# Optimization experiments

Hardware: AMD Instinct MI355X
Metric: run time of the kernel (lower is better)

The kernel has to match this reference:

```python
import jax, jax.numpy as jnp
import numpy as np
from jax import lax

B, T, C, H = 4, 2048, 1024, 16
K = C // H            # head size = 64
E_MIX, E_DEC = 32, 64  # TIME_MIX_EXTRA_DIM, TIME_DECAY_EXTRA_DIM
EPS = 1e-5 * 8**2      # GroupNorm eps with head_size_divisor=8


def setup_inputs() -> dict:
    key = jax.random.key(0)
    ks = jax.random.split(key, 24)
    u01 = lambda k, s: jax.random.uniform(k, s, jnp.float32, -0.01, 0.01)
    nrm = lambda k, s, sc: jax.random.normal(k, s, jnp.float32) * sc
    return {
        "x": jax.random.normal(ks[0], (B, T, C), jnp.float32),
        "time_maa_x": jax.random.uniform(ks[1], (1, 1, C)),
        "time_maa_w": jax.random.uniform(ks[2], (1, 1, C)),
        "time_maa_k": jax.random.uniform(ks[3], (1, 1, C)),
        "time_maa_v": jax.random.uniform(ks[4], (1, 1, C)),
        "time_maa_r": jax.random.uniform(ks[5], (1, 1, C)),
        "time_maa_g": jax.random.uniform(ks[6], (1, 1, C)),
        "maa_w1": u01(ks[7], (C, 5 * E_MIX)),
        "maa_w2": u01(ks[8], (5, E_MIX, C)),
        "time_decay": jax.random.uniform(ks[9], (1, 1, C), jnp.float32, -6.0, -1.0),
        "td_w1": u01(ks[10], (C, E_DEC)),
        "td_w2": u01(ks[11], (E_DEC, C)),
        "u": nrm(ks[12], (H, K), 0.1),   # time_faaaa
        "Wr": nrm(ks[13], (C, C), 0.02),
        "Wk": nrm(ks[14], (C, C), 0.02),
        "Wv": nrm(ks[15], (C, C), 0.02),
        "Wg": nrm(ks[16], (C, C), 0.02),
        "Wo": nrm(ks[17], (C, C), 0.02),
        "ln_g": jnp.ones((C,), jnp.float32),
        "ln_b": jnp.zeros((C,), jnp.float32),
    }


def _rwkv6_tmix(x, time_maa_x, time_maa_w, time_maa_k, time_maa_v, time_maa_r,
                time_maa_g, maa_w1, maa_w2, time_decay, td_w1, td_w2, u,
                Wr, Wk, Wv, Wg, Wo, ln_g, ln_b):
    b, t, c = x.shape
    # token shift: prepend zero row, drop last (ZeroPad2d((0,0,1,-1)))
    x_prev = jnp.pad(x, ((0, 0), (1, 0), (0, 0)))[:, :t]
    xx = x_prev - x
    # low-rank data-dependent mixing
    mix = jnp.tanh((x + xx * time_maa_x) @ maa_w1).reshape(b, t, 5, E_MIX)
    mix = jnp.einsum('btfe,fec->fbtc', mix, maa_w2)  # [5,B,T,C]
    mw, mk, mv, mr, mg = mix
    xw = x + xx * (time_maa_w + mw)
    xk = x + xx * (time_maa_k + mk)
    xv = x + xx * (time_maa_v + mv)
    xr = x + xx * (time_maa_r + mr)
    xg = x + xx * (time_maa_g + mg)
    r = xr @ Wr.T
    k = xk @ Wk.T
    v = xv @ Wv.T
    g = jax.nn.silu(xg @ Wg.T)
    w = time_decay + jnp.tanh(xw @ td_w1) @ td_w2
    decay = jnp.exp(-jnp.exp(w))  # per-channel decay in (0,1)

    # WKV6 linear recurrence, scan over time, vectorized over (B,H)
    to_tbhk = lambda a: a.reshape(b, t, H, K).transpose(1, 0, 2, 3)
    rs, ks_, vs, ds = map(to_tbhk, (r, k, v, decay))

    def step(S, inp):  # S: [B,H,K,K] (key x value)
        r_t, k_t, v_t, d_t = inp
        kv = k_t[..., :, None] * v_t[..., None, :]          # [B,H,K,K]
        y = jnp.einsum('bhk,bhkj->bhj', r_t, S + u[None, :, :, None] * kv)
        S = d_t[..., None] * S + kv
        return S, y

    S0 = jnp.zeros((b, H, K, K), x.dtype)
    _, y = lax.scan(step, S0, (rs, ks_, vs, ds))            # y: [T,B,H,K]
    y = y.transpose(1, 0, 2, 3)                             # [B,T,H,K]

    # GroupNorm over each head's K channels
    mu = y.mean(-1, keepdims=True)
    var = y.var(-1, keepdims=True)
    y = ((y - mu) / jnp.sqrt(var + EPS)).reshape(b, t, c) * ln_g + ln_b
    return (y * g) @ Wo.T


def reference(x, time_maa_x, time_maa_w, time_maa_k, time_maa_v, time_maa_r,
              time_maa_g, maa_w1, maa_w2, time_decay, td_w1, td_w2, u,
              Wr, Wk, Wv, Wg, Wo, ln_g, ln_b):
    return _rwkv6_tmix(x, time_maa_x, time_maa_w, time_maa_k, time_maa_v,
                       time_maa_r, time_maa_g, maa_w1, maa_w2, time_decay,
                       td_w1, td_w2, u, Wr, Wk, Wv, Wg, Wo, ln_g, ln_b)
```

## Files before the change

kernel.cpp:

```cpp
#include <hip/hip_runtime.h>

typedef unsigned int u32;
typedef unsigned short u16;
typedef __attribute__((ext_vector_type(8))) short short8;
typedef __attribute__((ext_vector_type(4))) float f32x4;

__device__ __forceinline__ float b2f(u16 h){ u32 x = ((u32)h) << 16; return __builtin_bit_cast(float, x); }
__device__ __forceinline__ u16 f2b(float f){
  u32 x = __builtin_bit_cast(u32, f);
  x += 0x7fffu + ((x >> 16) & 1u);
  return (u16)(x >> 16);
}
#define LOH(u) ((u16)((u) & 0xffffu))
#define HIH(u) ((u16)((u) >> 16))

__device__ __forceinline__ void gload16(const u16* g, u16* lds){
  __builtin_amdgcn_global_load_lds((const __attribute__((address_space(1))) u32*)g,
                                   (__attribute__((address_space(3))) u32*)lds, 16, 0, 0);
}

struct G4P { const u16* A[5]; const u16* B[5]; u16* C[5]; };

template<int MODE>
__global__ __launch_bounds__(256, 4) void gemm128_k(G4P gp, float* __restrict__ Cf)
{
  __shared__ u16 lds[16384];
  const int tid = threadIdx.x;
  const int z = blockIdx.z;
  if (MODE == 0 && z == 4 && blockIdx.y != 0) return;
  const u16* __restrict__ A  = gp.A[z];
  const u16* __restrict__ Bw = gp.B[z];
  const int wid = tid >> 6, lane = tid & 63;
  const int wr = wid >> 1, wc = wid & 1;
  const int l16 = lane & 15, kq = lane >> 4;
  const int swr = (l16 >> 1) & 3;
  const long row0 = (long)blockIdx.x * 128;
  const long col0 = (long)blockIdx.y * 128;

  f32x4 acc[4][4];
#pragma unroll
  for (int i = 0; i < 4; i++)
#pragma unroll
    for (int j = 0; j < 4; j++) acc[i][j] = (f32x4)0.0f;

  const int srow = tid >> 2;
  const int sk8 = ((tid & 3) ^ ((tid >> 3) & 3)) * 8;
  const u16* Agp = A  + (row0 + srow) * 1024 + sk8;
  const u16* Bgp = Bw + (col0 + srow) * 1024 + sk8;

  auto STAGE = [&](int buf, int kt){
    u16* Ab = lds + buf * 8192;
    u16* Bb = Ab + 4096;
    const int ko = kt * 32;
    gload16(Agp + ko,         Ab + tid * 8);
    gload16(Agp + 65536 + ko, Ab + (tid + 256) * 8);
    gload16(Bgp + ko,         Bb + tid * 8);
    gload16(Bgp + 65536 + ko, Bb + (tid + 256) * 8);
  };

  STAGE(0, 0);
  const int NT = 32;
  for (int t = 0; t < NT; t++){
    const int cur = t & 1;
    if (t + 1 < NT){
      STAGE(cur ^ 1, t + 1);
      asm volatile("s_waitcnt vmcnt(4)" ::: "memory");
    } else {
      asm volatile("s_waitcnt vmcnt(0)" ::: "memory");
    }
    __builtin_amdgcn_sched_barrier(0);
    __builtin_amdgcn_s_barrier();
    __builtin_amdgcn_sched_barrier(0);
    const u16* Ab = lds + cur * 8192;
    const u16* Bb = Ab + 4096;
    short8 afr[4], bfr[4];
#pragma unroll
    for (int ni = 0; ni < 4; ni++)
      bfr[ni] = *(const short8*)&Bb[(wc*64 + ni*16 + l16)*32 + (kq ^ swr)*8];
#pragma unroll
    for (int mi = 0; mi < 4; mi++)
      afr[mi] = *(const short8*)&Ab[(wr*64 + mi*16 + l16)*32 + (kq ^ swr)*8];
    __builtin_amdgcn_s_setprio(1);
#pragma unroll
    for (int mi = 0; mi < 4; mi++)
#pragma unroll
      for (int ni = 0; ni < 4; ni++)
        acc[mi][ni] = __builtin_amdgcn_mfma_f32_16x16x32_bf16(afr[mi], bfr[ni], acc[mi][ni], 0, 0, 0);
    __builtin_amdgcn_s_setprio(0);
    __builtin_amdgcn_s_barrier();
  }

  const bool SILU = (MODE == 0) && (z == 3);
  const bool TANH = (MODE == 0) && (z == 4);
  const int  ldc  = (MODE == 0 && z == 4) ? 128 : 1024;
#pragma unroll
  for (int mi = 0; mi < 4; mi++){
#pragma unroll
    for (int qq = 0; qq < 4; qq++){
      const long r = row0 + wr*64 + mi*16 + kq*4 + qq;
      if (MODE == 0){
        u16* crow = gp.C[z] + r * ldc + col0 + wc*64 + l16;
#pragma unroll
        for (int ni = 0; ni < 4; ni++){
          float v = acc[mi][ni][qq];
          if (SILU) v = v / (1.0f + expf(-v));
          if (TANH) v = tanhf(v);
          crow[ni * 16] = f2b(v);
        }
      } else {
        float* crow = Cf + r * 1024 + col0 + wc*64 + l16;
#pragma unroll
        for (int ni = 0; ni < 4; ni++)
          crow[ni * 16] = acc[mi][ni][qq];
      }
    }
  }
}

__global__ __launch_bounds__(256) void gemm_tanh(
    const u16* __restrict__ A, int lda,
    const u16* __restrict__ B, int ldb,
    u16* __restrict__ C, int ldc, int K)
{
  __shared__ u16 As[4096];
  __shared__ u16 Bs[4096];
  const int tid = threadIdx.x;
  const int wave = tid >> 6, lane = tid & 63;
  const int wr = wave >> 1, wc = wave & 1;
  const int l16 = lane & 15, kq = lane >> 4;
  const long row0 = (long)blockIdx.x * 128;
  const long col0 = (long)blockIdx.y * 128;

  f32x4 acc[4][4];
#pragma unroll
  for (int i = 0; i < 4; i++)
#pragma unroll
    for (int j = 0; j < 4; j++) acc[i][j] = (f32x4)0.0f;

  const int c0 = tid, c1 = tid + 256;
  const u16* Ag0 = A + (row0 + (c0 >> 2)) * (long)lda + (c0 & 3) * 8;
  const u16* Ag1 = A + (row0 + (c1 >> 2)) * (long)lda + (c1 & 3) * 8;
  const u16* Bg0 = B + (col0 + (c0 >> 2)) * (long)ldb + (c0 & 3) * 8;
  const u16* Bg1 = B + (col0 + (c1 >> 2)) * (long)ldb + (c1 & 3) * 8;
  u16* Al0 = &As[c0 * 8]; u16* Al1 = &As[c1 * 8];
  u16* Bl0 = &Bs[c0 * 8]; u16* Bl1 = &Bs[c1 * 8];

  for (int kk = 0; kk < K; kk += 32){
    __syncthreads();
    gload16(Ag0 + kk, Al0);
    gload16(Ag1 + kk, Al1);
    gload16(Bg0 + kk, Bl0);
    gload16(Bg1 + kk, Bl1);
    __syncthreads();
    short8 af[4], bfr[4];
#pragma unroll
    for (int mi = 0; mi < 4; mi++) af[mi]  = *(const short8*)&As[(wr*64 + mi*16 + l16)*32 + kq*8];
#pragma unroll
    for (int ni = 0; ni < 4; ni++) bfr[ni] = *(const short8*)&Bs[(wc*64 + ni*16 + l16)*32 + kq*8];
#pragma unroll
    for (int mi = 0; mi < 4; mi++)
#pragma unroll
      for (int ni = 0; ni < 4; ni++)
        acc[mi][ni] = __builtin_amdgcn_mfma_f32_16x16x32_bf16(af[mi], bfr[ni], acc[mi][ni], 0, 0, 0);
  }

#pragma unroll
  for (int mi = 0; mi < 4; mi++){
#pragma unroll
    for (int qq = 0; qq < 4; qq++){
      const long r = row0 + wr*64 + mi*16 + kq*4 + qq;
#pragma unroll
      for (int ni = 0; ni < 4; ni++){
        const long c = col0 + wc*64 + ni*16 + l16;
        C[r * ldc + c] = f2b(tanhf(acc[mi][ni][qq]));
      }
    }
  }
}

struct Mix5P { const u32* pxx; u16* out[5]; const float* tm[5]; };

__global__ __launch_bounds__(256) void gemm_mix5(
    const u16* __restrict__ Am, const u16* __restrict__ W2T, Mix5P mp)
{
  __shared__ u16 As[128 * 160];
  __shared__ u16 Bs[128 * 32];
  const int tid = threadIdx.x;
  const int wave = tid >> 6, lane = tid & 63;
  const int wr = wave >> 1, wc = wave & 1;
  const int l16 = lane & 15, kq = lane >> 4;
  const long row0 = (long)blockIdx.x * 128;
  const long col0 = (long)blockIdx.y * 128;

#pragma unroll
  for (int it = 0; it < 10; it++){
    const int c = tid + it * 256;
    const int r = c / 20, c8 = c - r * 20;
    gload16(Am + (row0 + r) * 256 + c8 * 8, &As[c * 8]);
  }

  u32 pxx[64];
#pragma unroll
  for (int mi = 0; mi < 4; mi++)
#pragma unroll
    for (int qq = 0; qq < 4; qq++){
      const long r = row0 + wr*64 + mi*16 + kq*4 + qq;
#pragma unroll
      for (int ni = 0; ni < 4; ni++){
        const long c = col0 + wc*64 + ni*16 + l16;
        pxx[mi*16 + qq*4 + ni] = mp.pxx[r * 1024 + c];
      }
    }

  for (int z = 0; z < 5; z++){
    __syncthreads();
    const u16* B = W2T + z * 32768;
#pragma unroll
    for (int it = 0; it < 2; it++){
      const int c = tid + it * 256;
      gload16(B + (col0 + (c >> 2)) * 32 + (c & 3) * 8, &Bs[c * 8]);
    }
    __syncthreads();
    short8 af[4], bfr[4];
#pragma unroll
    for (int mi = 0; mi < 4; mi++) af[mi]  = *(const short8*)&As[(wr*64 + mi*16 + l16)*160 + z*32 + kq*8];
#pragma unroll
    for (int ni = 0; ni < 4; ni++) bfr[ni] = *(const short8*)&Bs[(wc*64 + ni*16 + l16)*32 + kq*8];
    f32x4 acc[4][4];
#pragma unroll
    for (int i = 0; i < 4; i++)
#pragma unroll
      for (int j = 0; j < 4; j++) acc[i][j] = (f32x4)0.0f;
#pragma unroll
    for (int mi = 0; mi < 4; mi++)
#pragma unroll
      for (int ni = 0; ni < 4; ni++)
        acc[mi][ni] = __builtin_amdgcn_mfma_f32_16x16x32_bf16(af[mi], bfr[ni], acc[mi][ni], 0, 0, 0);

    const float* tm = mp.tm[z];
    float tmv[4];
#pragma unroll
    for (int ni = 0; ni < 4; ni++) tmv[ni] = tm[col0 + wc*64 + ni*16 + l16];
    u16* C = mp.out[z];
#pragma unroll
    for (int mi = 0; mi < 4; mi++){
#pragma unroll
      for (int qq = 0; qq < 4; qq++){
        const long r = row0 + wr*64 + mi*16 + kq*4 + qq;
        u16* crow = C + r * 1024 + col0 + wc*64 + l16;
#pragma unroll
        for (int ni = 0; ni < 4; ni++){
          const u32 pk = pxx[mi*16 + qq*4 + ni];
          const float xc = b2f(LOH(pk));
          const float xx = b2f(HIH(pk));
          crow[ni * 16] = f2b(xc + xx * (tmv[ni] + acc[mi][ni][qq]));
        }
      }
    }
  }
}

__global__ __launch_bounds__(256) void mkxm_k(const float* __restrict__ X,
    const float* __restrict__ tmx, u16* __restrict__ XM, u32* __restrict__ PXX)
{
  const long idx = (long)blockIdx.x * 256 + threadIdx.x;
  const long m = idx >> 8;
  const int c4 = (int)(idx & 255) * 4;
  const float4 x = *(const float4*)(X + m * 1024 + c4);
  float4 p = make_float4(0.f, 0.f, 0.f, 0.f);
  if ((m & 2047) != 0) p = *(const float4*)(X + (m - 1) * 1024 + c4);
  const float4 t = *(const float4*)(tmx + c4);
  ushort4 o;
  o.x = f2b(x.x + (p.x - x.x) * t.x);
  o.y = f2b(x.y + (p.y - x.y) * t.y);
  o.z = f2b(x.z + (p.z - x.z) * t.z);
  o.w = f2b(x.w + (p.w - x.w) * t.w);
  *(ushort4*)(XM + m * 1024 + c4) = o;
  uint4 px;
  px.x = (u32)f2b(x.x) | ((u32)f2b(p.x - x.x) << 16);
  px.y = (u32)f2b(x.y) | ((u32)f2b(p.y - x.y) << 16);
  px.z = (u32)f2b(x.z) | ((u32)f2b(p.z - x.z) << 16);
  px.w = (u32)f2b(x.w) | ((u32)f2b(p.w - x.w) << 16);
  *(uint4*)(PXX + m * 1024 + c4) = px;
}

struct PrepP { const float* s[5]; u16* d[5];
               const float* mw1; const float* mw2; const float* tdw1; const float* tdw2;
               u16* w1t; u16* w2t; u16* tw1t; u16* tw2t; };
__global__ __launch_bounds__(256) void prep_k(PrepP pp)
{
  const int y = blockIdx.y;
  const long idx = (long)blockIdx.x * 256 + threadIdx.x;
  if (y < 5){
    const float4 v = ((const float4*)pp.s[y])[idx];
    ushort4 o; o.x = f2b(v.x); o.y = f2b(v.y); o.z = f2b(v.z); o.w = f2b(v.w);
    ((ushort4*)pp.d[y])[idx] = o;
  } else if (y == 5){
    const int k = (int)(idx & 1023);
    const int n = (int)(idx >> 10);
    pp.w1t[idx] = (n < 160) ? f2b(pp.mw1[(long)k * 160 + n]) : (u16)0;
  } else if (y == 6){
    if (idx >= 163840) return;
    const int k = (int)(idx & 31);
    const int col = (int)(idx >> 5) & 1023;
    const int f = (int)(idx >> 15);
    pp.w2t[idx] = f2b(pp.mw2[f * 32768 + k * 1024 + col]);
  } else if (y == 7){
    if (idx >= 131072) return;
    const int k = (int)(idx & 1023);
    const int n = (int)(idx >> 10);
    pp.tw1t[idx] = (n < 64) ? f2b(pp.tdw1[(long)k * 64 + n]) : (u16)0;
  } else {
    if (idx >= 65536) return;
    const int k = (int)(idx & 63);
    const int n = (int)(idx >> 6);
    pp.tw2t[idx] = f2b(pp.tdw2[(long)k * 1024 + n]);
  }
}

__global__ __launch_bounds__(256) void wkv_s1(
    u16* __restrict__ Rg, const u16* __restrict__ Kg, const u16* __restrict__ Vg,
    const u16* __restrict__ Hbg, const u16* __restrict__ TW2Tg,
    const float* __restrict__ TDg, const float* __restrict__ Ug,
    u16* __restrict__ Yg, float* __restrict__ Ag, float* __restrict__ Pg)
{
  __shared__ u16 RT_[64 * 72];
  __shared__ u16 KT_[64 * 72];
  __shared__ u16 KTT_[64 * 72];
  __shared__ u16 V_[64 * 72];
  __shared__ u16 VT_[64 * 72];
  __shared__ char UD_[64 * 68 * 4];
  __shared__ float us_[64];
  __shared__ float td_[64];
  __shared__ float dg4_[256];
  __shared__ float dg_[64];
  float* D_ = (float*)UD_;
  u16*  M_  = (u16*)UD_;

  const int tid = threadIdx.x;
  const int bh = blockIdx.x >> 5, ch = blockIdx.x & 31;
  const int b = bh >> 4, h = bh & 15, cb = h * 64;
  const long rowb = (long)b * 2048 + ch * 64;

  if (tid < 64){ us_[tid] = Ug[cb + tid]; td_[tid] = TDg[cb + tid]; }

  const int iS = tid >> 2, sg = tid & 3;
  {
    const uint4* hsrc = (const uint4*)(Hbg + (rowb + iS) * 128 + sg * 16);
    uint4* hdst = (uint4*)&RT_[iS * 72 + sg * 16];
    hdst[0] = hsrc[0]; hdst[1] = hsrc[1];
    const uint4* wsrc = (const uint4*)(TW2Tg + (cb + iS) * 64 + sg * 16);
    uint4* wdst = (uint4*)&KT_[iS * 72 + sg * 16];
    wdst[0] = wsrc[0]; wdst[1] = wsrc[1];
  }
  __syncthreads();
  {
    const int wave = tid >> 6, lane = tid & 63;
    const int wr = wave >> 1, wc = wave & 1;
    const int l16 = lane & 15, kq = lane >> 4;
    f32x4 dacc[2][2];
#pragma unroll
    for (int a = 0; a < 2; a++)
#pragma unroll
      for (int c = 0; c < 2; c++) dacc[a][c] = (f32x4)0.0f;
#pragma unroll
    for (int ks = 0; ks < 2; ks++){
      short8 af[2], bf[2];
#pragma unroll
      for (int mi = 0; mi < 2; mi++) af[mi] = *(const short8*)&RT_[(wr*32 + mi*16 + l16)*72 + ks*32 + kq*8];
#pragma unroll
      for (int ni = 0; ni < 2; ni++) bf[ni] = *(const short8*)&KT_[(wc*32 + ni*16 + l16)*72 + ks*32 + kq*8];
#pragma unroll
      for (int mi = 0; mi < 2; mi++)
#pragma unroll
        for (int ni = 0; ni < 2; ni++)
          dacc[mi][ni] = __builtin_amdgcn_mfma_f32_16x16x32_bf16(af[mi], bf[ni], dacc[mi][ni], 0, 0, 0);
    }
    __syncthreads();
#pragma unroll
    for (int mi = 0; mi < 2; mi++)
#pragma unroll
      for (int ni = 0; ni < 2; ni++)
#pragma unroll
        for (int qq = 0; qq < 4; qq++){
          const int ii = wr*32 + mi*16 + kq*4 + qq;
          const int jj = wc*32 + ni*16 + l16;
          D_[ii * 68 + jj] = expf(-expf(dacc[mi][ni][qq] + td_[jj]));
        }
  }
  {
    const long go = (rowb + iS) * 1024 + cb + sg * 16;
    uint4 a0 = *(const uint4*)(Rg + go);
    uint4 a1 = *(const uint4*)(Rg + go + 8);
    u32* rd = (u32*)&RT_[iS * 72 + sg * 16];
    rd[0]=a0.x; rd[1]=a0.y; rd[2]=a0.z; rd[3]=a0.w;
    rd[4]=a1.x; rd[5]=a1.y; rd[6]=a1.z; rd[7]=a1.w;
    a0 = *(const uint4*)(Kg + go); a1 = *(const uint4*)(Kg + go + 8);
    u32* kd = (u32*)&KT_[iS * 72 + sg * 16];
    kd[0]=a0.x; kd[1]=a0.y; kd[2]=a0.z; kd[3]=a0.w;
    kd[4]=a1.x; kd[5]=a1.y; kd[6]=a1.z; kd[7]=a1.w;
    a0 = *(const uint4*)(Vg + go); a1 = *(const uint4*)(Vg + go + 8);
    u32* vd = (u32*)&V_[iS * 72 + sg * 16];
    vd[0]=a0.x; vd[1]=a0.y; vd[2]=a0.z; vd[3]=a0.w;
    vd[4]=a1.x; vd[5]=a1.y; vd[6]=a1.z; vd[7]=a1.w;
    const u32 vw[8] = {a0.x,a0.y,a0.z,a0.w,a1.x,a1.y,a1.z,a1.w};
#pragma unroll
    for (int e = 0; e < 8; e++){
      VT_[(sg*16 + 2*e    ) * 72 + iS] = LOH(vw[e]);
      VT_[(sg*16 + 2*e + 1) * 72 + iS] = HIH(vw[e]);
    }
  }
  __syncthreads();
  {
    const int i = tid & 63, q = tid >> 6;
    const u32* rr = (const u32*)&RT_[i * 72 + q * 16];
    const u32* kr = (const u32*)&KT_[i * 72 + q * 16];
    const float* up = &us_[q * 16];
    float ds = 0.0f;
#pragma unroll
    for (int e = 0; e < 8; e++){
      ds += b2f(LOH(rr[e])) * up[2*e]   * b2f(LOH(kr[e]));
      ds += b2f(HIH(rr[e])) * up[2*e+1] * b2f(HIH(kr[e]));
    }
    dg4_[i * 4 + q] = ds;
  }
  __syncthreads();
  if (tid < 64){
    const int k = tid;
    dg_[k] = dg4_[k*4] + dg4_[k*4+1] + dg4_[k*4+2] + dg4_[k*4+3];
    float pz = 1.0f;
#pragma unroll 4
    for (int i = 0; i < 64; i++){
      const float d = D_[i * 68 + k];
      const int ro = i * 72 + k;
      RT_[ro] = f2b(b2f(RT_[ro]) * pz);
      pz *= d;
      const u16 kb = f2b(b2f(KT_[ro]) * (1.0f / pz));
      KT_[ro] = kb;
      KTT_[k * 72 + i] = kb;
    }
    Pg[((long)bh * 32 + ch) * 64 + k] = pz;
  }
  __syncthreads();
  {
    const u32* rr = (const u32*)&RT_[iS * 72 + sg * 16];
    u32* out = (u32*)(Rg + (rowb + iS) * 1024 + cb + sg * 16);
#pragma unroll
    for (int e = 0; e < 8; e++) out[e] = rr[e];
  }
  const int wave = tid >> 6, lane = tid & 63;
  const int wr = wave >> 1, wc = wave & 1;
  const int l16 = lane & 15, kq = lane >> 4;
  {
    f32x4 acc[2][2];
#pragma unroll
    for (int a = 0; a < 2; a++)
#pragma unroll
      for (int c = 0; c < 2; c++) acc[a][c] = (f32x4)0.0f;
#pragma unroll
    for (int ks = 0; ks < 2; ks++){
      short8 af[2], bf[2];
#pragma unroll
      for (int mi = 0; mi < 2; mi++) af[mi] = *(const short8*)&RT_[(wr*32 + mi*16 + l16)*72 + ks*32 + kq*8];
#pragma unroll
      for (int ni = 0; ni < 2; ni++) bf[ni] = *(const short8*)&KT_[(wc*32 + ni*16 + l16)*72 + ks*32 + kq*8];
#pragma unroll
      for (int mi = 0; mi < 2; mi++)
#pragma unroll
        for (int ni = 0; ni < 2; ni++)
          acc[mi][ni] = __builtin_amdgcn_mfma_f32_16x16x32_bf16(af[mi], bf[ni], acc[mi][ni], 0, 0, 0);
    }
    __syncthreads();
#pragma unroll
    for (int mi = 0; mi < 2; mi++)
#pragma unroll
      for (int ni = 0; ni < 2; ni++)
#pragma unroll
        for (int qq = 0; qq < 4; qq++){
          const int ii = wr*32 + mi*16 + kq*4 + qq;
          const int ss = wc*32 + ni*16 + l16;
          M_[ii * 72 + ss] = f2b(ss < ii ? acc[mi][ni][qq] : 0.0f);
        }
  }
  __syncthreads();
  {
    f32x4 accY[2][2], accA[2][2];
#pragma unroll
    for (int a = 0; a < 2; a++)
#pragma unroll
      for (int c = 0; c < 2; c++){ accY[a][c] = (f32x4)0.0f; accA[a][c] = (f32x4)0.0f; }
#pragma unroll
    for (int ks = 0; ks < 2; ks++){
      short8 am[2], ak[2], bv[2];
#pragma unroll
      for (int mi = 0; mi < 2; mi++){
        am[mi] = *(const short8*)&M_[(wr*32 + mi*16 + l16)*72 + ks*32 + kq*8];
        ak[mi] = *(const short8*)&KTT_[(wr*32 + mi*16 + l16)*72 + ks*32 + kq*8];
      }
#pragma unroll
      for (int ni = 0; ni < 2; ni++) bv[ni] = *(const short8*)&VT_[(wc*32 + ni*16 + l16)*72 + ks*32 + kq*8];
#pragma unroll
      for (int mi = 0; mi < 2; mi++)
#pragma unroll
        for (int ni = 0; ni < 2; ni++){
          accY[mi][ni] = __builtin_amdgcn_mfma_f32_16x16x32_bf16(am[mi], bv[ni], accY[mi][ni], 0, 0, 0);
          accA[mi][ni] = __builtin_amdgcn_mfma_f32_16x16x32_bf16(ak[mi], bv[ni], accA[mi][ni], 0, 0, 0);
        }
    }
    float* abase = Ag + ((long)bh * 32 + ch) * 4096;
#pragma unroll
    for (int mi = 0; mi < 2; mi++)
#pragma unroll
      for (int qq = 0; qq < 4; qq++){
        const int ii = wr*32 + mi*16 + kq*4 + qq;
        u16* yrow = Yg + (rowb + ii) * 1024 + cb;
        float* arow = abase + ii * 64;
#pragma unroll
        for (int ni = 0; ni < 2; ni++){
          const int jj = wc*32 + ni*16 + l16;
          const float yv = accY[mi][ni][qq] + dg_[ii] * b2f(V_[ii * 72 + jj]);
          yrow[jj] = f2b(yv);
          arow[jj] = accA[mi][ni][qq];
        }
      }
  }
}

__global__ __launch_bounds__(256) void wkv_s2(
    const float* __restrict__ Ag, const float* __restrict__ Pg, float* __restrict__ Sg)
{
  const int tid = threadIdx.x;
  const int bh = blockIdx.x >> 2, kq = blockIdx.x & 3;
  const int kk = tid >> 4, jo = tid & 15;
  const int krow = kq * 16 + kk;
  const long base = (long)bh * 32;
  float4 S = make_float4(0.f, 0.f, 0.f, 0.f);
  for (int g = 0; g < 4; g++){
    float4 a[8]; float ps[8];
#pragma unroll
    for (int j = 0; j < 8; j++){
      const long c = base + g * 8 + j;
      a[j]  = *(const float4*)(Ag + c * 4096 + krow * 64 + jo * 4);
      ps[j] = Pg[c * 64 + krow];
    }
#pragma unroll
    for (int j = 0; j < 8; j++){
      const long mo = (base + g * 8 + j) * 4096 + krow * 64 + jo * 4;
      *(float4*)(Sg + mo) = S;
      S.x = ps[j] * (S.x + a[j].x); S.y = ps[j] * (S.y + a[j].y);
      S.z = ps[j] * (S.z + a[j].z); S.w = ps[j] * (S.w + a[j].w);
    }
  }
}

__global__ __launch_bounds__(256) void wkv_s3g(
    const u16* __restrict__ Rtg, const float* __restrict__ Sg,
    const u16* __restrict__ Yg, const u16* __restrict__ G,
    const float* __restrict__ lng, const float* __restrict__ lnb,
    u16* __restrict__ Z)
{
  __shared__ float Ss[4096];
  __shared__ u16 RTs[64 * 66];
  __shared__ float red1[256], red2[256];
  const int tid = threadIdx.x;
  const int bh = blockIdx.x >> 5, ch = blockIdx.x & 31;
  const int b = bh >> 4, h = bh & 15, cb = h * 64;
  const long rowb = (long)b * 2048 + ch * 64;
  const bool CROSS = (ch != 0);

  if (CROSS){
    const float4* sp = (const float4*)(Sg + ((long)bh * 32 + ch) * 4096);
    float4* sd = (float4*)Ss;
#pragma unroll
    for (int e = 0; e < 4; e++) sd[tid + e * 256] = sp[tid + e * 256];
    const int iS = tid >> 2, sg4 = tid & 3;
    const u32* src = (const u32*)(Rtg + (rowb + iS) * 1024 + cb + sg4 * 16);
    u32* dst = (u32*)&RTs[iS * 66 + sg4 * 16];
#pragma unroll
    for (int e = 0; e < 8; e++) dst[e] = src[e];
  }
  __syncthreads();

  const int i_ = tid & 63, q = tid >> 6, jb = q * 16;
  float y[16];
  {
    const u32* yp = (const u32*)(Yg + (rowb + i_) * 1024 + cb + jb);
#pragma unroll
    for (int j2 = 0; j2 < 8; j2++){
      const u32 u = yp[j2];
      y[2*j2] = b2f(LOH(u)); y[2*j2+1] = b2f(HIH(u));
    }
  }
  if (CROSS){
    float rt[64];
    const u32* rr = (const u32*)&RTs[i_ * 66];
#pragma unroll
    for (int kk = 0; kk < 32; kk++){
      const u32 u = rr[kk];
      rt[2*kk] = b2f(LOH(u)); rt[2*kk+1] = b2f(HIH(u));
    }
#pragma unroll
    for (int k = 0; k < 64; k++){
      const float rk = rt[k];
      const float4* sr = (const float4*)&Ss[k * 64 + jb];
#pragma unroll
      for (int j4 = 0; j4 < 4; j4++){
        const float4 sv = sr[j4];
        y[4*j4+0] += rk*sv.x; y[4*j4+1] += rk*sv.y; y[4*j4+2] += rk*sv.z; y[4*j4+3] += rk*sv.w;
      }
    }
  }
  float s = 0.0f, sq = 0.0f;
#pragma unroll
  for (int j = 0; j < 16; j++){ s += y[j]; sq += y[j]*y[j]; }
  red1[q * 64 + i_] = s;
  red2[q * 64 + i_] = sq;
  __syncthreads();
  const float St = red1[i_] + red1[64 + i_] + red1[128 + i_] + red1[192 + i_];
  const float Qt = red2[i_] + red2[64 + i_] + red2[128 + i_] + red2[192 + i_];
  const float mean = St * 0.015625f;
  const float var = Qt * 0.015625f - mean * mean;
  const float rstd = rsqrtf(var + 6.4e-4f);

  const u32* gp = (const u32*)(G + (rowb + i_) * 1024 + cb + jb);
  const float4* lgp = (const float4*)(lng + cb + jb);
  const float4* lbp = (const float4*)(lnb + cb + jb);
  u32* zo = (u32*)(Z + (rowb + i_) * 1024 + cb + jb);
#pragma unroll
  for (int j4 = 0; j4 < 4; j4++){
    const float4 lg = lgp[j4];
    const float4 lb = lbp[j4];
    const u32 g01 = gp[2*j4], g23 = gp[2*j4+1];
    const float z0 = ((y[4*j4+0]-mean)*rstd*lg.x + lb.x) * b2f(LOH(g01));
    const float z1 = ((y[4*j4+1]-mean)*rstd*lg.y + lb.y) * b2f(HIH(g01));
    const float z2 = ((y[4*j4+2]-mean)*rstd*lg.z + lb.z) * b2f(LOH(g23));
    const float z3 = ((y[4*j4+3]-mean)*rstd*lg.w + lb.w) * b2f(HIH(g23));
    zo[2*j4]   = (u32)f2b(z0) | ((u32)f2b(z1) << 16);
    zo[2*j4+1] = (u32)f2b(z2) | ((u32)f2b(z3) << 16);
  }
}

extern "C" void kernel_launch(void* const* d_in, const int* in_sizes, int n_in,
                              void* d_out, int out_size, void* d_ws, size_t ws_size,
                              hipStream_t stream)
{
  (void)in_sizes; (void)n_in; (void)out_size; (void)ws_size;
  const float* X    = (const float*)d_in[0];
  const float* TMX  = (const float*)d_in[1];
  const float* TMW  = (const float*)d_in[2];
  const float* TMK  = (const float*)d_in[3];
  const float* TMV  = (const float*)d_in[4];
  const float* TMR  = (const float*)d_in[5];
  const float* TMG  = (const float*)d_in[6];
  const float* MW1  = (const float*)d_in[7];
  const float* MW2  = (const float*)d_in[8];
  const float* TD   = (const float*)d_in[9];
  const float* TDW1 = (const float*)d_in[10];
  const float* TDW2 = (const float*)d_in[11];
  const float* U    = (const float*)d_in[12];
  const float* WR   = (const float*)d_in[13];
  const float* WK   = (const float*)d_in[14];
  const float* WV   = (const float*)d_in[15];
  const float* WG   = (const float*)d_in[16];
  const float* WO   = (const float*)d_in[17];
  const float* LNG  = (const float*)d_in[18];
  const float* LNB  = (const float*)d_in[19];

  char* ws = (char*)d_ws;
  const size_t SLOT = 16777216ULL;
  u16* S1 = (u16*)(ws + 0 * SLOT);
  u16* S2 = (u16*)(ws + 1 * SLOT);
  u16* S3 = (u16*)(ws + 2 * SLOT);
  u16* S4 = (u16*)(ws + 3 * SLOT);
  u16* S5 = (u16*)(ws + 4 * SLOT);
  u16* S6 = (u16*)(ws + 5 * SLOT);
  u16* S7 = (u16*)(ws + 6 * SLOT);
  u16* S8 = (u16*)(ws + 7 * SLOT);
  u16* S9 = (u16*)(ws + 8 * SLOT);
  char* p = ws + 9 * SLOT;
  auto alloc = [&](size_t bytes) -> void* {
    void* q = p; p += (bytes + 255) & ~(size_t)255; return q;
  };
  u16* MIXB = (u16*)alloc(8192ULL * 256 * 2);
  u16* Hb   = (u16*)alloc(8192ULL * 128 * 2);
  u16* W1T  = (u16*)alloc(256ULL * 1024 * 2);
  u16* W2T  = (u16*)alloc(5ULL * 1024 * 32 * 2);
  u16* TW1T = (u16*)alloc(128ULL * 1024 * 2);
  u16* TW2T = (u16*)alloc(1024ULL * 64 * 2);
  u16* WRb  = (u16*)alloc(1048576ULL * 2);
  u16* WKb  = (u16*)alloc(1048576ULL * 2);
  u16* WVb  = (u16*)alloc(1048576ULL * 2);
  u16* WGb  = (u16*)alloc(1048576ULL * 2);
  u16* WOb  = (u16*)alloc(1048576ULL * 2);
  float* Ab = (float*)alloc(33554432ULL);
  float* Pg = (float*)alloc(524288ULL);

  u16*   XM = S1; u16* XW = S2; u16* XK = S3; u16* XV = S4; u16* XR = S5; u16* XG = S6;
  u32*   PXX = (u32*)S7;
  u16*   Rb = S1; u16* Kb = S7; u16* Vb = S8; u16* Gb = S9;
  u16*   Y   = S2;
  float* Sg  = (float*)S7;
  u16*   Z   = S4;

  PrepP pp;
  pp.s[0]=WR; pp.s[1]=WK; pp.s[2]=WV; pp.s[3]=WG; pp.s[4]=WO;
  pp.d[0]=WRb; pp.d[1]=WKb; pp.d[2]=WVb; pp.d[3]=WGb; pp.d[4]=WOb;
  pp.mw1 = MW1; pp.mw2 = MW2; pp.tdw1 = TDW1; pp.tdw2 = TDW2;
  pp.w1t = W1T; pp.w2t = W2T; pp.tw1t = TW1T; pp.tw2t = TW2T;
  prep_k<<<dim3(1024, 9), 256, 0, stream>>>(pp);

  mkxm_k<<<8192, 256, 0, stream>>>(X, TMX, XM, PXX);

  gemm_tanh<<<dim3(64, 2), 256, 0, stream>>>(XM, 1024, W1T, 1024, MIXB, 256, 1024);

  Mix5P mp;
  mp.pxx = PXX;
  mp.out[0]=XW; mp.out[1]=XK; mp.out[2]=XV; mp.out[3]=XR; mp.out[4]=XG;
  mp.tm[0]=TMW; mp.tm[1]=TMK; mp.tm[2]=TMV; mp.tm[3]=TMR; mp.tm[4]=TMG;
  gemm_mix5<<<dim3(64, 8), 256, 0, stream>>>(MIXB, W2T, mp);

  G4P gp;
  gp.A[0]=XR; gp.A[1]=XK; gp.A[2]=XV; gp.A[3]=XG; gp.A[4]=XW;
  gp.B[0]=WRb; gp.B[1]=WKb; gp.B[2]=WVb; gp.B[3]=WGb; gp.B[4]=TW1T;
  gp.C[0]=Rb; gp.C[1]=Kb; gp.C[2]=Vb; gp.C[3]=Gb; gp.C[4]=Hb;
  gemm128_k<0><<<dim3(64, 8, 5), 256, 0, stream>>>(gp, nullptr);

  wkv_s1<<<2048, 256, 0, stream>>>(Rb, Kb, Vb, Hb, TW2T, TD, U, Y, Ab, Pg);
  wkv_s2<<<256, 256, 0, stream>>>(Ab, Pg, Sg);
  wkv_s3g<<<2048, 256, 0, stream>>>(Rb, Sg, Y, Gb, LNG, LNB, Z);

  G4P go;
  go.A[0]=Z; go.B[0]=WOb; go.C[0]=nullptr;
  gemm128_k<1><<<dim3(64, 8, 1), 256, 0, stream>>>(go, (float*)d_out);
}
```

Before: 288.1 us.

## Merge weight prep with token-shift kernel and parallelize decay cumprod across waves

Folds the token-shift/mix kernel into the weight-conversion prep kernel as extra grid rows, removing one launch and letting the two independent workloads share the GPU. In wkv_s1, the serial 64-step decay cumulative product that ran on only 64 threads is split into four 16-step segments handled by all 256 threads, with segment prefix products exchanged through shared memory. This shortens the serial critical path per block at the cost of an extra barrier and a small shared buffer, and changes float rounding order slightly.

Result: faster. 275.0 us (-4.5%).

```diff
diff --git a/kernel.cpp b/kernel.cpp
--- a/kernel.cpp
+++ b/kernel.cpp
@@ -260,62 +260,61 @@
   }
 }
 
-__global__ __launch_bounds__(256) void mkxm_k(const float* __restrict__ X,
-    const float* __restrict__ tmx, u16* __restrict__ XM, u32* __restrict__ PXX)
+struct PrepMkP { const float* s[5]; u16* d[5];
+                 const float* mw1; const float* mw2; const float* tdw1; const float* tdw2;
+                 u16* w1t; u16* w2t; u16* tw1t; u16* tw2t;
+                 const float* X; const float* tmx; u16* XM; u32* PXX; };
+__global__ __launch_bounds__(256) void prepmk_k(PrepMkP pp)
 {
-  const long idx = (long)blockIdx.x * 256 + threadIdx.x;
+  const int y = blockIdx.y;
+  if (y < 9){
+    const long idx = (long)blockIdx.x * 256 + threadIdx.x;
+    if (y < 5){
+      const float4 v = ((const float4*)pp.s[y])[idx];
+      ushort4 o; o.x = f2b(v.x); o.y = f2b(v.y); o.z = f2b(v.z); o.w = f2b(v.w);
+      ((ushort4*)pp.d[y])[idx] = o;
+    } else if (y == 5){
+      const int k = (int)(idx & 1023);
+      const int n = (int)(idx >> 10);
+      pp.w1t[idx] = (n < 160) ? f2b(pp.mw1[(long)k * 160 + n]) : (u16)0;
+    } else if (y == 6){
+      if (idx >= 163840) return;
+      const int k = (int)(idx & 31);
+      const int col = (int)(idx >> 5) & 1023;
+      const int f = (int)(idx >> 15);
+      pp.w2t[idx] = f2b(pp.mw2[f * 32768 + k * 1024 + col]);
+    } else if (y == 7){
+      if (idx >= 131072) return;
+      const int k = (int)(idx & 1023);
+      const int n = (int)(idx >> 10);
+      pp.tw1t[idx] = (n < 64) ? f2b(pp.tdw1[(long)k * 64 + n]) : (u16)0;
+    } else {
+      if (idx >= 65536) return;
+      const int k = (int)(idx & 63);
+      const int n = (int)(idx >> 6);
+      pp.tw2t[idx] = f2b(pp.tdw2[(long)k * 1024 + n]);
+    }
+    return;
+  }
+  const long idx = (((long)(y - 9) * 1024 + blockIdx.x) * 256 + threadIdx.x);
   const long m = idx >> 8;
   const int c4 = (int)(idx & 255) * 4;
-  const float4 x = *(const float4*)(X + m * 1024 + c4);
+  const float4 x = *(const float4*)(pp.X + m * 1024 + c4);
   float4 p = make_float4(0.f, 0.f, 0.f, 0.f);
-  if ((m & 2047) != 0) p = *(const float4*)(X + (m - 1) * 1024 + c4);
-  const float4 t = *(const float4*)(tmx + c4);
+  if ((m & 2047) != 0) p = *(const float4*)(pp.X + (m - 1) * 1024 + c4);
+  const float4 t = *(const float4*)(pp.tmx + c4);
   ushort4 o;
   o.x = f2b(x.x + (p.x - x.x) * t.x);
   o.y = f2b(x.y + (p.y - x.y) * t.y);
   o.z = f2b(x.z + (p.z - x.z) * t.z);
   o.w = f2b(x.w + (p.w - x.w) * t.w);
-  *(ushort4*)(XM + m * 1024 + c4) = o;
+  *(ushort4*)(pp.XM + m * 1024 + c4) = o;
   uint4 px;
   px.x = (u32)f2b(x.x) | ((u32)f2b(p.x - x.x) << 16);
   px.y = (u32)f2b(x.y) | ((u32)f2b(p.y - x.y) << 16);
   px.z = (u32)f2b(x.z) | ((u32)f2b(p.z - x.z) << 16);
   px.w = (u32)f2b(x.w) | ((u32)f2b(p.w - x.w) << 16);
-  *(uint4*)(PXX + m * 1024 + c4) = px;
-}
-
-struct PrepP { const float* s[5]; u16* d[5];
-               const float* mw1; const float* mw2; const float* tdw1; const float* tdw2;
-               u16* w1t; u16* w2t; u16* tw1t; u16* tw2t; };
-__global__ __launch_bounds__(256) void prep_k(PrepP pp)
-{
-  const int y = blockIdx.y;
-  const long idx = (long)blockIdx.x * 256 + threadIdx.x;
-  if (y < 5){
-    const float4 v = ((const float4*)pp.s[y])[idx];
-    ushort4 o; o.x = f2b(v.x); o.y = f2b(v.y); o.z = f2b(v.z); o.w = f2b(v.w);
-    ((ushort4*)pp.d[y])[idx] = o;
-  } else if (y == 5){
-    const int k = (int)(idx & 1023);
-    const int n = (int)(idx >> 10);
-    pp.w1t[idx] = (n < 160) ? f2b(pp.mw1[(long)k * 160 + n]) : (u16)0;
-  } else if (y == 6){
-    if (idx >= 163840) return;
-    const int k = (int)(idx & 31);
-    const int col = (int)(idx >> 5) & 1023;
-    const int f = (int)(idx >> 15);
-    pp.w2t[idx] = f2b(pp.mw2[f * 32768 + k * 1024 + col]);
-  } else if (y == 7){
-    if (idx >= 131072) return;
-    const int k = (int)(idx & 1023);
-    const int n = (int)(idx >> 10);
-    pp.tw1t[idx] = (n < 64) ? f2b(pp.tdw1[(long)k * 64 + n]) : (u16)0;
-  } else {
-    if (idx >= 65536) return;
-    const int k = (int)(idx & 63);
-    const int n = (int)(idx >> 6);
-    pp.tw2t[idx] = f2b(pp.tdw2[(long)k * 1024 + n]);
-  }
+  *(uint4*)(pp.PXX + m * 1024 + c4) = px;
 }
 
 __global__ __launch_bounds__(256) void wkv_s1(
@@ -334,6 +333,7 @@
   __shared__ float td_[64];
   __shared__ float dg4_[256];
   __shared__ float dg_[64];
+  __shared__ float segp_[256];
   float* D_ = (float*)UD_;
   u16*  M_  = (u16*)UD_;
 
@@ -425,21 +425,29 @@
     dg4_[i * 4 + q] = ds;
   }
   __syncthreads();
-  if (tid < 64){
-    const int k = tid;
-    dg_[k] = dg4_[k*4] + dg4_[k*4+1] + dg4_[k*4+2] + dg4_[k*4+3];
+  {
+    const int k = tid & 63, seg = tid >> 6;
+    if (seg == 0) dg_[k] = dg4_[k*4] + dg4_[k*4+1] + dg4_[k*4+2] + dg4_[k*4+3];
+    const int i0 = seg * 16;
+    float lp = 1.0f;
+#pragma unroll
+    for (int i = 0; i < 16; i++) lp *= D_[(i0 + i) * 68 + k];
+    segp_[seg * 64 + k] = lp;
+    __syncthreads();
     float pz = 1.0f;
-#pragma unroll 4
-    for (int i = 0; i < 64; i++){
-      const float d = D_[i * 68 + k];
-      const int ro = i * 72 + k;
+    for (int s = 0; s < seg; s++) pz *= segp_[s * 64 + k];
+#pragma unroll
+    for (int i = 0; i < 16; i++){
+      const int ii = i0 + i;
+      const float d = D_[ii * 68 + k];
+      const int ro = ii * 72 + k;
       RT_[ro] = f2b(b2f(RT_[ro]) * pz);
       pz *= d;
       const u16 kb = f2b(b2f(KT_[ro]) * (1.0f / pz));
       KT_[ro] = kb;
-      KTT_[k * 72 + i] = kb;
-    }
-    Pg[((long)bh * 32 + ch) * 64 + k] = pz;
+      KTT_[k * 72 + ii] = kb;
+    }
+    if (seg == 3) Pg[((long)bh * 32 + ch) * 64 + k] = pz;
   }
   __syncthreads();
   {
@@ -702,14 +710,13 @@
   float* Sg  = (float*)S7;
   u16*   Z   = S4;
 
-  PrepP pp;
+  PrepMkP pp;
   pp.s[0]=WR; pp.s[1]=WK; pp.s[2]=WV; pp.s[3]=WG; pp.s[4]=WO;
   pp.d[0]=WRb; pp.d[1]=WKb; pp.d[2]=WVb; pp.d[3]=WGb; pp.d[4]=WOb;
   pp.mw1 = MW1; pp.mw2 = MW2; pp.tdw1 = TDW1; pp.tdw2 = TDW2;
   pp.w1t = W1T; pp.w2t = W2T; pp.tw1t = TW1T; pp.tw2t = TW2T;
-  prep_k<<<dim3(1024, 9), 256, 0, stream>>>(pp);
-
-  mkxm_k<<<8192, 256, 0, stream>>>(X, TMX, XM, PXX);
+  pp.X = X; pp.tmx = TMX; pp.XM = XM; pp.PXX = PXX;
+  prepmk_k<<<dim3(1024, 17), 256, 0, stream>>>(pp);
 
   gemm_tanh<<<dim3(64, 2), 256, 0, stream>>>(XM, 1024, W1T, 1024, MIXB, 256, 1024);
 
```
